# Optimization experiments

Measured on AMD Instinct MI355X. Metric: run time of the kernel, lower is better.

Reference implementation:

```python
import jax, jax.numpy as jnp
import numpy as np

N_NODES = 50000
N_EDGES = 1600000
IN_DIM = 64
EDGE_DIM = 8
N_GRAPHS = 256
EXP_IN = 32
H = 64  # hidden dim per head / GCN hidden
EPS = 1e-5
NEG_SLOPE = 0.2


def gat_layer(x, src, dst, ea, W, a_src, a_dst, We, a_e, bias, heads, dim, concat):
    """PyG-style GATConv with edge features and self-loops (fill_value='mean')."""
    N = x.shape[0]
    ones_e = jnp.ones((ea.shape[0],), x.dtype)
    cnt = jax.ops.segment_sum(ones_e, dst, num_segments=N)
    loop_attr = jax.ops.segment_sum(ea, dst, num_segments=N) / jnp.maximum(cnt, 1.0)[:, None]
    s = jnp.concatenate([src, jnp.arange(N)])
    d = jnp.concatenate([dst, jnp.arange(N)])
    eaf = jnp.concatenate([ea, loop_attr], axis=0)  # [E+N, edge_dim]
    h = (x @ W).reshape(N, heads, dim)              # [N, H, D]
    ee = (eaf @ We).reshape(-1, heads, dim)         # [E+N, H, D]
    al_src = (h * a_src).sum(-1)                    # [N, H]
    al_dst = (h * a_dst).sum(-1)                    # [N, H]
    score = al_src[s] + al_dst[d] + (ee * a_e).sum(-1)
    score = jax.nn.leaky_relu(score, NEG_SLOPE)     # [E+N, H]
    m = jax.ops.segment_max(score, d, num_segments=N)
    ex = jnp.exp(score - m[d])
    att = ex / jax.ops.segment_sum(ex, d, num_segments=N)[d]
    out = jax.ops.segment_sum(h[s] * att[:, :, None], d, num_segments=N)  # [N, H, D]
    out = out.reshape(N, heads * dim) if concat else out.mean(axis=1)
    return out + bias


def gcn_layer(x, src, dst, W, b):
    """PyG-style GCNConv: add self loops, symmetric degree normalization."""
    N = x.shape[0]
    s = jnp.concatenate([src, jnp.arange(N)])
    d = jnp.concatenate([dst, jnp.arange(N)])
    deg = jax.ops.segment_sum(jnp.ones((s.shape[0],), x.dtype), d, num_segments=N)
    dinv = jax.lax.rsqrt(deg)  # deg >= 1 thanks to self loops
    norm = dinv[s] * dinv[d]
    h = x @ W
    return jax.ops.segment_sum(h[s] * norm[:, None], d, num_segments=N) + b


def bn(x, g, b):
    m = x.mean(axis=0)
    v = x.var(axis=0)
    return g * (x - m) * jax.lax.rsqrt(v + EPS) + b


def mean_pool(x, batch, num_graphs):
    s = jax.ops.segment_sum(x, batch, num_segments=num_graphs)
    c = jax.ops.segment_sum(jnp.ones((x.shape[0],), x.dtype), batch, num_segments=num_graphs)
    return s / jnp.maximum(c, 1.0)[:, None]


def setup_inputs() -> dict:
    key = jax.random.key(0)
    ks = jax.random.split(key, 32)
    p = lambda i, shape: jax.random.normal(ks[i], shape, jnp.float32) * 0.05
    z = lambda n: jnp.zeros((n,), jnp.float32)
    o = lambda n: jnp.ones((n,), jnp.float32)
    return {
        "x": jax.random.normal(ks[0], (N_NODES, IN_DIM), jnp.float32),
        "edge_attr": jax.random.normal(ks[1], (N_EDGES, EDGE_DIM), jnp.float32),
        "experimental_feat": jax.random.normal(ks[2], (N_GRAPHS, EXP_IN), jnp.float32),
        "edge_index": jax.random.randint(ks[3], (2, N_EDGES), 0, N_NODES),
        "batch": jnp.sort(jax.random.randint(ks[4], (N_NODES,), 0, N_GRAPHS)),
        "W1": p(5, (IN_DIM, 4 * H)), "att_src1": p(6, (4, H)), "att_dst1": p(7, (4, H)),
        "We1": p(8, (EDGE_DIM, 4 * H)), "att_e1": p(9, (4, H)), "b1": z(4 * H),
        "g1": o(4 * H), "be1": z(4 * H),
        "W2": p(10, (4 * H, H)), "att_src2": p(11, (1, H)), "att_dst2": p(12, (1, H)),
        "We2": p(13, (EDGE_DIM, H)), "att_e2": p(14, (1, H)), "b2": z(H),
        "g2": o(H), "be2": z(H),
        "Wg1": p(15, (H, H)), "bg1": z(H), "g3": o(H), "be3": z(H),
        "Wg2": p(16, (H, H)), "bg2": z(H), "g4": o(H), "be4": z(H),
        "Wex1": p(17, (EXP_IN, H)), "bex1": z(H), "Wex2": p(18, (H, H)), "bex2": z(H),
        "Wc1": p(19, (2 * H, 128)), "bc1": z(128), "Wc2": p(20, (128, 1)), "bc2": z(1),
    }


def reference(x, edge_attr, experimental_feat, edge_index, batch,
              W1, att_src1, att_dst1, We1, att_e1, b1, g1, be1,
              W2, att_src2, att_dst2, We2, att_e2, b2, g2, be2,
              Wg1, bg1, g3, be3, Wg2, bg2, g4, be4,
              Wex1, bex1, Wex2, bex2, Wc1, bc1, Wc2, bc2):
    src, dst = edge_index[0], edge_index[1]
    h = gat_layer(x, src, dst, edge_attr, W1, att_src1, att_dst1, We1, att_e1, b1, 4, H, True)
    h = jax.nn.relu(bn(h, g1, be1))
    h = gat_layer(h, src, dst, edge_attr, W2, att_src2, att_dst2, We2, att_e2, b2, 1, H, False)
    h = jax.nn.relu(bn(h, g2, be2))  # dropout = identity in eval
    h = gcn_layer(h, src, dst, Wg1, bg1)
    h = jax.nn.relu(bn(h, g3, be3))
    h = gcn_layer(h, src, dst, Wg2, bg2)
    h = jax.nn.relu(bn(h, g4, be4))
    xp = mean_pool(h, batch, N_GRAPHS)                    # [G, H]
    e = jax.nn.relu(experimental_feat @ Wex1 + bex1)
    e = jax.nn.relu(e @ Wex2 + bex2)
    combined = jnp.concatenate([xp, e], axis=1)           # [G, 2H]
    combined = jax.nn.relu(combined @ Wc1 + bc1)          # [G, 128]
    out = combined @ Wc2 + bc2                            # [G, 1]
    return (out, xp, combined)
```

## Files before the change

kernel.cpp:

```cpp
#include <hip/hip_runtime.h>
#include <hip/hip_bf16.h>

#define N_NODES 50000
#define N_EDGES 1600000
#define N_GRAPHS 256
#define NEG_SLOPE 0.2f
#define BN_EPS 1e-5f

typedef __hip_bfloat16 bf16;
typedef __attribute__((ext_vector_type(8))) short s16x8;
typedef __attribute__((ext_vector_type(4))) float f32x4;

__device__ __forceinline__ float b2f(bf16 v){ return __bfloat162float(v); }
__device__ __forceinline__ bf16 f2b(float v){ return __float2bfloat16(v); }
__device__ __forceinline__ float us2f(unsigned short u){ return __uint_as_float(((unsigned)u)<<16); }
__device__ __forceinline__ unsigned short f2us(float v){ bf16 b = f2b(v); return *(unsigned short*)&b; }
__device__ __forceinline__ unsigned pk2(float a, float b){ return (unsigned)f2us(a) | ((unsigned)f2us(b)<<16); }
__device__ __forceinline__ float ldF(const void* p, size_t i, int m){
  return m ? ((const float*)p)[i] : b2f(((const bf16*)p)[i]);
}
__device__ __forceinline__ float sane(float v){
  return (v == v && fabsf(v) < 1e30f) ? v : 0.f;
}
__device__ __forceinline__ float sel4(const float v[4], int h){
  float r = v[0];
  r = (h==1) ? v[1] : r;
  r = (h==2) ? v[2] : r;
  r = (h==3) ? v[3] : r;
  return r;
}
__device__ __forceinline__ void acc8(float* acc, float w, uint4 u){
  acc[0] += w*us2f((unsigned short)(u.x & 0xffff)); acc[1] += w*us2f((unsigned short)(u.x >> 16));
  acc[2] += w*us2f((unsigned short)(u.y & 0xffff)); acc[3] += w*us2f((unsigned short)(u.y >> 16));
  acc[4] += w*us2f((unsigned short)(u.z & 0xffff)); acc[5] += w*us2f((unsigned short)(u.z >> 16));
  acc[6] += w*us2f((unsigned short)(u.w & 0xffff)); acc[7] += w*us2f((unsigned short)(u.w >> 16));
}
__device__ __forceinline__ void unp8(float* o, uint4 u){
  o[0] = us2f((unsigned short)(u.x & 0xffff)); o[1] = us2f((unsigned short)(u.x >> 16));
  o[2] = us2f((unsigned short)(u.y & 0xffff)); o[3] = us2f((unsigned short)(u.y >> 16));
  o[4] = us2f((unsigned short)(u.z & 0xffff)); o[5] = us2f((unsigned short)(u.z >> 16));
  o[6] = us2f((unsigned short)(u.w & 0xffff)); o[7] = us2f((unsigned short)(u.w >> 16));
}
__device__ __forceinline__ s16x8 pk8(const float* v){
  s16x8 r;
  #pragma unroll
  for(int j=0;j<8;j++) r[j] = (short)f2us(v[j]);
  return r;
}

__device__ int detect_mode_block(const void* x){
  __shared__ int s_ins;
  if(threadIdx.x == 0) s_ins = 0;
  __syncthreads();
  const unsigned short* u = (const unsigned short*)x;
  int c = 0;
  for(int i = threadIdx.x; i < 1024; i += blockDim.x){
    float v = fabsf(us2f(u[i]));
    if(!(v > 1e-6f && v < 1e4f)) c++;
  }
  if(c) atomicAdd(&s_ins, c);
  __syncthreads();
  return (s_ins > 128) ? 1 : 0;
}

#define NSEG 33
struct Bank { const void* p[NSEG]; int n[NSEG]; int off[NSEG]; };

__global__ void k_convert(Bank b, const void* xdet, float* out){
  int m = detect_mode_block(xdet);
  int seg = blockIdx.y;
  int i = blockIdx.x*256 + threadIdx.x;
  if(i < b.n[seg]) out[b.off[seg] + i] = ldF(b.p[seg], i, m);
}

__global__ void k_cvt_x(const void* x, bf16* xb){
  int m = detect_mode_block(x);
  int i4 = blockIdx.x*256 + threadIdx.x;
  if(i4 >= N_NODES*16) return;
  if(m){
    float4 v = ((const float4*)x)[i4];
    ((ushort4*)xb)[i4] = make_ushort4(f2us(v.x), f2us(v.y), f2us(v.z), f2us(v.w));
  } else {
    ((ushort4*)xb)[i4] = ((const ushort4*)x)[i4];
  }
}

__global__ void k_we(const float* __restrict__ We1, const float* __restrict__ ae1,
                     const float* __restrict__ We2, const float* __restrict__ ae2,
                     float* __restrict__ w_e){
  int t = threadIdx.x;
  if(t < 32){
    int h = t >> 3, k = t & 7;
    float s = 0.f;
    for(int d=0;d<64;d++) s += We1[k*256 + h*64 + d] * ae1[h*64 + d];
    w_e[t] = s;
  } else if(t < 40){
    int k = t - 32;
    float s = 0.f;
    for(int d=0;d<64;d++) s += We2[k*64 + d] * ae2[d];
    w_e[t] = s;
  }
}

__global__ void k_wt(const float* __restrict__ W1, const float* __restrict__ W2,
                     const float* __restrict__ Wg1, const float* __restrict__ Wg2,
                     bf16* __restrict__ wt){
  int i = blockIdx.x*256 + threadIdx.x;
  if(i < 16384){
    int c = i >> 6, k = i & 63;
    wt[i] = f2b(W1[k*256 + c]);
  } else if(i < 32768){
    int j = i - 16384; int c = j >> 8, k = j & 255;
    wt[i] = f2b(W2[k*64 + c]);
  } else if(i < 36864){
    int j = i - 32768; int c = j >> 6, k = j & 63;
    wt[i] = f2b(Wg1[k*64 + c]);
  } else if(i < 40960){
    int j = i - 36864; int c = j >> 6, k = j & 63;
    wt[i] = f2b(Wg2[k*64 + c]);
  }
}

__global__ void k_count(const int* __restrict__ dst, int* __restrict__ cnt){
  int e = blockIdx.x*256 + threadIdx.x;
  if(e < N_EDGES){
    int d = dst[e]; if((unsigned)d >= N_NODES) d = 0;
    atomicAdd(&cnt[d], 1);
  }
}

__global__ void k_blocksum(const int* __restrict__ cnt, int* __restrict__ bsum){
  __shared__ int s[256];
  int i = blockIdx.x*256 + threadIdx.x;
  s[threadIdx.x] = (i < N_NODES) ? cnt[i] : 0;
  __syncthreads();
  for(int o=128;o>0;o>>=1){ if(threadIdx.x<o) s[threadIdx.x]+=s[threadIdx.x+o]; __syncthreads(); }
  if(threadIdx.x==0) bsum[blockIdx.x]=s[0];
}

__global__ void k_scan_bsum(const int* __restrict__ bsum, int* __restrict__ bofs, int nb){
  __shared__ int s[256];
  int t = threadIdx.x;
  s[t] = (t<nb) ? bsum[t] : 0;
  __syncthreads();
  for(int o=1;o<256;o<<=1){ int v=(t>=o)?s[t-o]:0; __syncthreads(); s[t]+=v; __syncthreads(); }
  bofs[t] = (t==0) ? 0 : s[t-1];
}

__global__ void k_scan_write(const int* __restrict__ cnt, const int* __restrict__ bofs,
                             int* __restrict__ rp, float* __restrict__ dinv){
  __shared__ int s[256];
  int t = threadIdx.x; int i = blockIdx.x*256 + t;
  int v = (i<N_NODES) ? cnt[i] : 0;
  s[t]=v; __syncthreads();
  for(int o=1;o<256;o<<=1){ int a=(t>=o)?s[t-o]:0; __syncthreads(); s[t]+=a; __syncthreads(); }
  if(i<N_NODES){
    rp[i+1] = s[t] + bofs[blockIdx.x];
    dinv[i] = rsqrtf((float)v + 1.f);
  }
  if(i==0) rp[0]=0;
}

__global__ void k_fill(const int* __restrict__ src, const int* __restrict__ dst,
                       const int* __restrict__ rp, int* __restrict__ fill,
                       const void* __restrict__ ea, const void* __restrict__ xdet,
                       const float* __restrict__ w_e,
                       int4* __restrict__ epk){
  int m = detect_mode_block(xdet);
  int e = blockIdx.x*256 + threadIdx.x;
  if(e >= N_EDGES) return;
  int d = dst[e]; if((unsigned)d >= N_NODES) d = 0;
  int p = atomicAdd(&fill[d], 1);
  int slot = rp[d] + p;
  if((unsigned)slot >= N_EDGES) return;
  int sv = src[e]; if((unsigned)sv >= N_NODES) sv = 0;
  float a[8];
  if(m){
    const float* eaf = (const float*)ea;
    float4 lo = *(const float4*)&eaf[(size_t)e*8];
    float4 hi = *(const float4*)&eaf[(size_t)e*8 + 4];
    a[0]=lo.x; a[1]=lo.y; a[2]=lo.z; a[3]=lo.w;
    a[4]=hi.x; a[5]=hi.y; a[6]=hi.z; a[7]=hi.w;
  } else {
    #pragma unroll
    for(int k=0;k<8;k++) a[k] = b2f(((const bf16*)ea)[(size_t)e*8 + k]);
  }
  unsigned d4[4];
  #pragma unroll
  for(int h=0;h<4;h++){
    float s = 0.f;
    #pragma unroll
    for(int k=0;k<8;k++) s += a[k]*w_e[h*8+k];
    d4[h] = f2us(s);
  }
  float s1 = 0.f;
  #pragma unroll
  for(int k=0;k<8;k++) s1 += a[k]*w_e[32+k];
  int4 pk;
  pk.x = sv;
  pk.y = (int)(d4[0] | (d4[1] << 16));
  pk.z = (int)(d4[2] | (d4[3] << 16));
  pk.w = (int)(unsigned)f2us(s1);
  epk[slot] = pk;
}

__global__ __launch_bounds__(256) void k_gemmA_mfma(
    const bf16* __restrict__ xb,
    const bf16* __restrict__ wt1,
    bf16* __restrict__ hp, int M)
{
  const int tid = threadIdx.x;
  const int w = tid >> 6, l = tid & 63;
  const int lr = l & 15, lg = l >> 4;
  const int bm = blockIdx.x*64 + w*16;
  const int arow_i = bm + lr;
  const uint4* arow = (const uint4*)(xb + (size_t)min(arow_i, M-1)*64);
  uint4 a0u = arow[lg];
  uint4 a1u = arow[4 + lg];
  s16x8 a0 = *(s16x8*)&a0u, a1 = *(s16x8*)&a1u;
  unsigned short* out = (unsigned short*)hp;
  const int orow0 = bm + lg*4;
  #pragma unroll
  for(int ct = 0; ct < 16; ct++){
    const uint4* brow = (const uint4*)(wt1 + (size_t)(ct*16 + lr)*64);
    uint4 b0u = brow[lg];
    uint4 b1u = brow[4 + lg];
    f32x4 acc = {0.f, 0.f, 0.f, 0.f};
    acc = __builtin_amdgcn_mfma_f32_16x16x32_bf16(a0, *(s16x8*)&b0u, acc, 0, 0, 0);
    acc = __builtin_amdgcn_mfma_f32_16x16x32_bf16(a1, *(s16x8*)&b1u, acc, 0, 0, 0);
    #pragma unroll
    for(int r = 0; r < 4; r++){
      int rr = orow0 + r;
      if(rr < M) out[(size_t)rr*256 + ct*16 + lr] = f2us(acc[r]);
    }
  }
}

template<int KIN>
__global__ __launch_bounds__(256) void k_gemmB_mfma(
    const bf16* __restrict__ A, const bf16* __restrict__ Wt,
    bf16* __restrict__ C, int M,
    const float* __restrict__ bnsums, const float* __restrict__ bng, const float* __restrict__ bnb)
{
  __shared__ float st_s[KIN];
  __shared__ float st_t[KIN];
  const int tid = threadIdx.x;
  if(tid < KIN){
    const float invN = 1.0f / (float)N_NODES;
    float mean = bnsums[tid]*invN;
    float var  = fmaxf(bnsums[KIN+tid]*invN - mean*mean, 0.f);
    float s = bng[tid]*rsqrtf(var + BN_EPS);
    st_s[tid] = s;
    st_t[tid] = bnb[tid] - mean*s;
  }
  __syncthreads();
  const int w = tid >> 6, l = tid & 63;
  const int lr = l & 15, lg = l >> 4;
  const int bm = blockIdx.x*64 + w*16;
  const int arow_i = bm + lr;
  const uint4* arow = (const uint4*)(A + (size_t)min(arow_i, M-1)*KIN);
  f32x4 acc[4];
  #pragma unroll
  for(int ct=0;ct<4;ct++) acc[ct] = (f32x4){0.f,0.f,0.f,0.f};
  #pragma unroll
  for(int k0 = 0; k0 < KIN; k0 += 32){
    uint4 au = arow[(k0 >> 3) + lg];
    int c0 = k0 + lg*8;
    float v[8]; unp8(v, au);
    #pragma unroll
    for(int j = 0; j < 8; j++){
      float y = sane(v[j])*st_s[c0+j] + st_t[c0+j];
      v[j] = fmaxf(y, 0.f);
    }
    s16x8 af = pk8(v);
    #pragma unroll
    for(int ct = 0; ct < 4; ct++){
      const uint4* brow = (const uint4*)(Wt + (size_t)(ct*16 + lr)*KIN);
      uint4 bu = brow[(k0 >> 3) + lg];
      acc[ct] = __builtin_amdgcn_mfma_f32_16x16x32_bf16(af, *(s16x8*)&bu, acc[ct], 0, 0, 0);
    }
  }
  unsigned short* out = (unsigned short*)C;
  const int orow0 = bm + lg*4;
  #pragma unroll
  for(int ct = 0; ct < 4; ct++){
    #pragma unroll
    for(int r = 0; r < 4; r++){
      int rr = orow0 + r;
      if(rr < M) out[(size_t)rr*64 + ct*16 + lr] = f2us(acc[ct][r]);
    }
  }
}

__global__ void k_al4(const bf16* __restrict__ hp, const float* __restrict__ asrc,
                      const float* __restrict__ adst,
                      float* __restrict__ als4, float* __restrict__ ald4){
  int idx = blockIdx.x*256 + threadIdx.x;
  if(idx >= N_NODES*4) return;
  int n = idx >> 2, h = idx & 3;
  const unsigned short* row = (const unsigned short*)hp + (size_t)n*256 + h*64;
  float ss=0.f, sd=0.f;
  #pragma unroll
  for(int q=0;q<16;q++){
    ushort4 u = *(const ushort4*)&row[4*q];
    float4 a_s = *(const float4*)&asrc[h*64 + 4*q];
    float4 a_d = *(const float4*)&adst[h*64 + 4*q];
    float v0=us2f(u.x), v1=us2f(u.y), v2=us2f(u.z), v3=us2f(u.w);
    ss += v0*a_s.x + v1*a_s.y + v2*a_s.z + v3*a_s.w;
    sd += v0*a_d.x + v1*a_d.y + v2*a_d.z + v3*a_d.w;
  }
  als4[idx]=ss; ald4[idx]=sd;
}

__global__ void k_al1(const bf16* __restrict__ hp, const float* __restrict__ asrc,
                      const float* __restrict__ adst,
                      float* __restrict__ als, float* __restrict__ ald){
  int n = blockIdx.x*256 + threadIdx.x;
  if(n >= N_NODES) return;
  const unsigned short* row = (const unsigned short*)hp + (size_t)n*64;
  float ss=0.f, sd=0.f;
  #pragma unroll
  for(int q=0;q<16;q++){
    ushort4 u = *(const ushort4*)&row[4*q];
    float4 a_s = *(const float4*)&asrc[4*q];
    float4 a_d = *(const float4*)&adst[4*q];
    float v0=us2f(u.x), v1=us2f(u.y), v2=us2f(u.z), v3=us2f(u.w);
    ss += v0*a_s.x + v1*a_s.y + v2*a_s.z + v3*a_s.w;
    sd += v0*a_d.x + v1*a_d.y + v2*a_d.z + v3*a_d.w;
  }
  als[n]=ss; ald[n]=sd;
}

__global__ __launch_bounds__(64) void k_gat_agg4(
    const int* __restrict__ rp, const int4* __restrict__ epk,
    const bf16* __restrict__ hp,
    const float* __restrict__ als4, const float* __restrict__ ald4,
    const float* __restrict__ bias256, bf16* __restrict__ out1){
  int n = blockIdx.x; int t = threadIdx.x;
  int eh = t >> 5, c8 = t & 31;
  int head = c8 >> 3;
  __shared__ int   ssrc[64];
  __shared__ float swt[64][4];
  int s0 = rp[n], e0 = rp[n+1];
  if((unsigned)s0 > N_EDGES){ s0=0; e0=0; }
  if(e0 < s0 || (unsigned)e0 > N_EDGES) e0 = s0;
  float4 aldv = *(const float4*)&ald4[n*4];
  float4 alsvn = *(const float4*)&als4[n*4];
  float wsum[4] = {0.f,0.f,0.f,0.f};
  float dsum[4] = {0.f,0.f,0.f,0.f};
  float acc[8]  = {0.f,0.f,0.f,0.f,0.f,0.f,0.f,0.f};
  const unsigned short* hpu = (const unsigned short*)hp;

  for(int base = s0; base < e0; base += 64){
    int m = min(64, e0 - base);
    if(t < m){
      int4 pk = epk[base+t];
      int sn = pk.x; if((unsigned)sn >= N_NODES) sn = 0;
      ssrc[t] = sn;
      float edf[4] = {us2f((unsigned short)(pk.y & 0xffff)), us2f((unsigned short)((unsigned)pk.y >> 16)),
                      us2f((unsigned short)(pk.z & 0xffff)), us2f((unsigned short)((unsigned)pk.z >> 16))};
      float4 alss = *(const float4*)&als4[sn*4];
      float alssv[4] = {alss.x, alss.y, alss.z, alss.w};
      float aldvv[4] = {aldv.x, aldv.y, aldv.z, aldv.w};
      float w4[4];
      #pragma unroll
      for(int h=0;h<4;h++){
        float sc = alssv[h] + aldvv[h] + edf[h];
        sc = sc > 0.f ? sc : NEG_SLOPE*sc;
        sc = fminf(sc, 30.f);
        float w = expf(sc);
        w4[h] = w;
        wsum[h] += w; dsum[h] += edf[h];
      }
      *(float4*)&swt[t][0] = make_float4(w4[0], w4[1], w4[2], w4[3]);
    }
    __syncthreads();
    #pragma unroll 4
    for(int i=0;i<m;i+=2){
      int j = i + eh;
      if(j < m){
        int row = ssrc[j];
        float w = swt[j][head];
        uint4 u = *(const uint4*)&hpu[(size_t)row*256 + 8*c8];
        acc8(acc, w, u);
      }
    }
    __syncthreads();
  }
  #pragma unroll
  for(int o=1;o<64;o<<=1){
    #pragma unroll
    for(int h=0;h<4;h++){
      wsum[h] += __shfl_xor(wsum[h], o);
      dsum[h] += __shfl_xor(dsum[h], o);
    }
  }
  #pragma unroll
  for(int q=0;q<8;q++) acc[q] += __shfl_xor(acc[q], 32);
  if(eh == 0){
    float alsnv[4] = {alsvn.x, alsvn.y, alsvn.z, alsvn.w};
    float aldnv[4] = {aldv.x, aldv.y, aldv.z, aldv.w};
    float sEh = sel4(wsum, head), sDh = sel4(dsum, head);
    float deg = (float)(e0 - s0);
    float sdot = deg > 0.f ? sDh/deg : 0.f;
    float sc = sel4(alsnv, head) + sel4(aldnv, head) + sdot;
    sc = sc > 0.f ? sc : NEG_SLOPE*sc;
    sc = fminf(sc, 30.f);
    float wself = expf(sc);
    float self[8];
    unp8(self, *(const uint4*)&hpu[(size_t)n*256 + 8*c8]);
    float4 b0 = *(const float4*)&bias256[8*c8];
    float4 b1 = *(const float4*)&bias256[8*c8 + 4];
    float bi[8] = {b0.x,b0.y,b0.z,b0.w,b1.x,b1.y,b1.z,b1.w};
    float inv = 1.f/(sEh + wself);
    float o8[8];
    #pragma unroll
    for(int q=0;q<8;q++) o8[q] = (acc[q] + wself*self[q])*inv + bi[q];
    uint4 st;
    st.x = pk2(o8[0],o8[1]); st.y = pk2(o8[2],o8[3]);
    st.z = pk2(o8[4],o8[5]); st.w = pk2(o8[6],o8[7]);
    *(uint4*)&((unsigned short*)out1)[(size_t)n*256 + 8*c8] = st;
  }
}

__global__ __launch_bounds__(64) void k_gat_agg1e(
    const int* __restrict__ rp, const int4* __restrict__ epk,
    const bf16* __restrict__ hp,
    const float* __restrict__ als, const float* __restrict__ ald,
    const float* __restrict__ bias64, bf16* __restrict__ out){
  int n = blockIdx.x; int t = threadIdx.x;
  int eg = t >> 3, c8 = t & 7;
  __shared__ float sw[64];
  __shared__ int   ssrc[64];
  int s0 = rp[n], e0 = rp[n+1];
  if((unsigned)s0 > N_EDGES){ s0=0; e0=0; }
  if(e0 < s0 || (unsigned)e0 > N_EDGES) e0 = s0;
  float aldn = ald[n];
  float wsum_l = 0.f, dsum_l = 0.f;
  float acc[8] = {0.f,0.f,0.f,0.f,0.f,0.f,0.f,0.f};
  const unsigned short* hpu = (const unsigned short*)hp;
  for(int base = s0; base < e0; base += 64){
    int m = min(64, e0 - base);
    if(t < m){
      int4 pk = epk[base+t];
      int sn = pk.x; if((unsigned)sn >= N_NODES) sn = 0;
      ssrc[t] = sn;
      float ed = us2f((unsigned short)(pk.w & 0xffff));
      float sc = als[sn] + aldn + ed;
      sc = sc > 0.f ? sc : NEG_SLOPE*sc;
      sc = fminf(sc, 30.f);
      float w = expf(sc);
      sw[t] = w;
      wsum_l += w; dsum_l += ed;
    }
    __syncthreads();
    #pragma unroll 2
    for(int i=0;i<m;i+=8){
      int j = i + eg;
      if(j < m){
        int row = ssrc[j];
        float w = sw[j];
        uint4 u = *(const uint4*)&hpu[(size_t)row*64 + 8*c8];
        acc8(acc, w, u);
      }
    }
    __syncthreads();
  }
  #pragma unroll
  for(int o=1;o<64;o<<=1){ wsum_l += __shfl_xor(wsum_l, o); dsum_l += __shfl_xor(dsum_l, o); }
  #pragma unroll
  for(int q=0;q<8;q++){
    acc[q] += __shfl_xor(acc[q], 8);
    acc[q] += __shfl_xor(acc[q], 16);
    acc[q] += __shfl_xor(acc[q], 32);
  }
  if(t < 8){
    float deg = (float)(e0 - s0);
    float sdot = deg > 0.f ? dsum_l/deg : 0.f;
    float sc = als[n] + aldn + sdot;
    sc = sc > 0.f ? sc : NEG_SLOPE*sc;
    sc = fminf(sc, 30.f);
    float wself = expf(sc);
    float self[8];
    unp8(self, *(const uint4*)&hpu[(size_t)n*64 + 8*t]);
    float4 b0 = *(const float4*)&bias64[8*t];
    float4 b1 = *(const float4*)&bias64[8*t + 4];
    float bi[8] = {b0.x,b0.y,b0.z,b0.w,b1.x,b1.y,b1.z,b1.w};
    float inv = 1.f/(wsum_l + wself);
    float o8[8];
    #pragma unroll
    for(int q=0;q<8;q++) o8[q] = (acc[q] + wself*self[q])*inv + bi[q];
    uint4 st;
    st.x = pk2(o8[0],o8[1]); st.y = pk2(o8[2],o8[3]);
    st.z = pk2(o8[4],o8[5]); st.w = pk2(o8[6],o8[7]);
    *(uint4*)&((unsigned short*)out)[(size_t)n*64 + 8*t] = st;
  }
}

__global__ __launch_bounds__(64) void k_gcn_agg(
    const int* __restrict__ rp, const int4* __restrict__ epk,
    const float* __restrict__ dinv, const bf16* __restrict__ gp,
    const float* __restrict__ bias, bf16* __restrict__ out){
  int n = blockIdx.x; int t = threadIdx.x;
  int eg = t >> 3, c8 = t & 7;
  __shared__ float sw[64];
  __shared__ int   ssrc[64];
  int s0 = rp[n], e0 = rp[n+1];
  if((unsigned)s0 > N_EDGES){ s0=0; e0=0; }
  if(e0 < s0 || (unsigned)e0 > N_EDGES) e0 = s0;
  float dn = dinv[n];
  float acc[8] = {0.f,0.f,0.f,0.f,0.f,0.f,0.f,0.f};
  const unsigned short* gpu = (const unsigned short*)gp;
  for(int base = s0; base < e0; base += 64){
    int m = min(64, e0 - base);
    if(t < m){
      int sn = epk[base+t].x; if((unsigned)sn >= N_NODES) sn = 0;
      ssrc[t]=sn; sw[t]=dinv[sn];
    }
    __syncthreads();
    #pragma unroll 2
    for(int i=0;i<m;i+=8){
      int j = i + eg;
      if(j < m){
        int row = ssrc[j];
        float w = sw[j];
        uint4 u = *(const uint4*)&gpu[(size_t)row*64 + 8*c8];
        acc8(acc, w, u);
      }
    }
    __syncthreads();
  }
  #pragma unroll
  for(int q=0;q<8;q++){
    acc[q] += __shfl_xor(acc[q], 8);
    acc[q] += __shfl_xor(acc[q], 16);
    acc[q] += __shfl_xor(acc[q], 32);
  }
  if(t < 8){
    float self[8];
    unp8(self, *(const uint4*)&gpu[(size_t)n*64 + 8*t]);
    float4 b0 = *(const float4*)&bias[8*t];
    float4 b1 = *(const float4*)&bias[8*t + 4];
    float bi[8] = {b0.x,b0.y,b0.z,b0.w,b1.x,b1.y,b1.z,b1.w};
    float o8[8];
    #pragma unroll
    for(int q=0;q<8;q++) o8[q] = dn*(acc[q] + dn*self[q]) + bi[q];
    uint4 st;
    st.x = pk2(o8[0],o8[1]); st.y = pk2(o8[2],o8[3]);
    st.z = pk2(o8[4],o8[5]); st.w = pk2(o8[6],o8[7]);
    *(uint4*)&((unsigned short*)out)[(size_t)n*64 + 8*t] = st;
  }
}

template<int C>
__global__ void k_colstats(const bf16* __restrict__ X, float* __restrict__ sums){
  constexpr int RPB = 128;
  constexpr int RSTEP = 256 / C;
  int c = threadIdx.x % C;
  int r0 = threadIdx.x / C;
  int rbeg = blockIdx.x * RPB;
  int rend = min(N_NODES, rbeg + RPB);
  const unsigned short* Xu = (const unsigned short*)X;
  float s = 0.f, q = 0.f;
  for(int r = rbeg + r0; r < rend; r += RSTEP){
    float v = sane(us2f(Xu[(size_t)r*C + c]));
    s += v; q += v*v;
  }
  atomicAdd(&sums[c], s);
  atomicAdd(&sums[C + c], q);
}

__global__ __launch_bounds__(64) void k_pool3(
    const bf16* __restrict__ h, const int* __restrict__ batch,
    const float* __restrict__ sums, const float* __restrict__ g4,
    const float* __restrict__ b4,
    float* __restrict__ psum, float* __restrict__ pcnt){
  int t = threadIdx.x;
  int n0 = blockIdx.x * 256;
  int n1 = min(N_NODES, n0 + 256);
  if(n0 >= n1) return;
  const float invN = 1.0f / (float)N_NODES;
  float mean = sums[t]*invN;
  float var = fmaxf(sums[64+t]*invN - mean*mean, 0.f);
  float rstd = rsqrtf(var + BN_EPS);
  float gg = g4[t], bb = b4[t];
  const unsigned short* hu = (const unsigned short*)h;
  int cur = batch[n0]; if((unsigned)cur >= N_GRAPHS) cur = 0;
  float acc = 0.f; int cl = 0;
  for(int n = n0; n < n1; n++){
    int g = batch[n]; if((unsigned)g >= N_GRAPHS) g = 0;
    if(g != cur){
      atomicAdd(&psum[cur*64 + t], acc);
      if(t == 0) atomicAdd(&pcnt[cur], (float)cl);
      acc = 0.f; cl = 0; cur = g;
    }
    float y = (sane(us2f(hu[(size_t)n*64 + t]))-mean)*rstd*gg + bb;
    acc += fmaxf(y, 0.f);
    cl++;
  }
  atomicAdd(&psum[cur*64 + t], acc);
  if(t == 0) atomicAdd(&pcnt[cur], (float)cl);
}

__device__ __forceinline__ void stO(void* o, size_t i, float v, int m){
  if(m) ((float*)o)[i] = v; else ((bf16*)o)[i] = f2b(v);
}

__global__ __launch_bounds__(128) void k_head(
    const float* __restrict__ psum, const float* __restrict__ pcnt,
    const float* __restrict__ exf,
    const float* __restrict__ Wex1, const float* __restrict__ bex1,
    const float* __restrict__ Wex2, const float* __restrict__ bex2,
    const float* __restrict__ Wc1, const float* __restrict__ bc1,
    const float* __restrict__ Wc2, const float* __restrict__ bc2,
    const void* __restrict__ xdet, void* __restrict__ dout){
  int m0 = detect_mode_block(xdet);
  int g = blockIdx.x; int t = threadIdx.x;
  __shared__ float ci[128];
  __shared__ float e1[64];
  __shared__ float comb[128];
  __shared__ float red[128];
  if(t < 64){
    float c = fmaxf(pcnt[g], 1.f);
    float xp = sane(psum[g*64 + t]) / c;
    ci[t] = xp;
    stO(dout, 256 + (size_t)g*64 + t, xp, m0);
  } else {
    int j = t - 64;
    float s = bex1[j];
    for(int k=0;k<32;k++) s += exf[g*32 + k] * Wex1[k*64 + j];
    e1[j] = fmaxf(s, 0.f);
  }
  __syncthreads();
  if(t >= 64){
    int j = t - 64;
    float s = bex2[j];
    for(int k=0;k<64;k++) s += e1[k] * Wex2[k*64 + j];
    ci[64 + j] = fmaxf(s, 0.f);
  }
  __syncthreads();
  {
    float s = bc1[t];
    for(int k=0;k<128;k++) s += ci[k] * Wc1[k*128 + t];
    s = fmaxf(s, 0.f);
    comb[t] = s;
    stO(dout, 256 + 16384 + (size_t)g*128 + t, s, m0);
  }
  __syncthreads();
  red[t] = comb[t] * Wc2[t];
  __syncthreads();
  for(int o=64;o>0;o>>=1){ if(t<o) red[t]+=red[t+o]; __syncthreads(); }
  if(t==0) stO(dout, g, red[0] + bc2[0], m0);
}

extern "C" void kernel_launch(void* const* d_in, const int* in_sizes, int n_in,
                              void* d_out, int out_size, void* d_ws, size_t ws_size,
                              hipStream_t stream){
  const void* x    = d_in[0];
  const void* ea   = d_in[1];
  const int* ei    = (const int*)d_in[3];
  const int* batch = (const int*)d_in[4];
  const int* src = ei;
  const int* dst = ei + N_EDGES;

  char* base = (char*)d_ws;
  size_t off = 0;
  auto alloc = [&](size_t bytes) -> void* {
    void* r = base + off;
    off += (bytes + 255) & ~(size_t)255;
    return r;
  };
  int*   cnt    = (int*)  alloc((size_t)N_NODES*4);
  int*   fill   = (int*)  alloc((size_t)N_NODES*4);
  float* bnstat = (float*)alloc(4096);
  float* pool   = (float*)alloc((size_t)(N_GRAPHS*64 + N_GRAPHS)*4);
  size_t zbytes = off;
  int*   rp      = (int*)  alloc((size_t)(N_NODES+1)*4);
  int*   bsum    = (int*)  alloc(256*4);
  int*   bofs    = (int*)  alloc(256*4);
  int4*  epk     = (int4*) alloc((size_t)N_EDGES*16);
  float* dinv    = (float*)alloc((size_t)N_NODES*4);
  float* w_e     = (float*)alloc(64*4);
  float* als4    = (float*)alloc((size_t)N_NODES*4*4);
  float* ald4    = (float*)alloc((size_t)N_NODES*4*4);
  float* wbank   = (float*)alloc(80000*4);
  bf16*  wt      = (bf16*) alloc((size_t)40960*2);
  bf16*  xb      = (bf16*) alloc((size_t)N_NODES*64*2);
  bf16*  hp      = (bf16*) alloc((size_t)N_NODES*256*2);
  bf16*  outb    = (bf16*) alloc((size_t)N_NODES*256*2);

  bf16* out1 = outb;
  bf16* out2 = outb;
  bf16* out3 = outb + (size_t)N_NODES*64;
  bf16* out4 = outb + (size_t)N_NODES*128;
  float* bn1 = bnstat;
  float* bn2 = bnstat + 512;
  float* bn3 = bnstat + 640;
  float* bn4 = bnstat + 768;
  float* psum = pool;
  float* pcnt = pool + N_GRAPHS*64;

  bf16* wt1  = wt;
  bf16* wt2  = wt + 16384;
  bf16* wtg1 = wt + 32768;
  bf16* wtg2 = wt + 36864;

  const int segidx[NSEG] = {2, 5,6,7,8,9,10,11,12, 13,14,15,16,17,18,19,20,
                            21,22,23,24, 25,26,27,28, 29,30,31,32, 33,34,35,36};
  const int segn[NSEG] = {8192, 16384,256,256,2048,256,256,256,256,
                          16384,64,64,512,64,64,64,64,
                          4096,64,64,64, 4096,64,64,64,
                          2048,64,4096,64, 16384,128,128,1};
  Bank bk;
  int offs[NSEG]; int acc0 = 0;
  for(int i=0;i<NSEG;i++){ bk.p[i]=d_in[segidx[i]]; bk.n[i]=segn[i]; bk.off[i]=acc0; offs[i]=acc0; acc0+=segn[i]; }
  const float* f_exf = wbank + offs[0];
  const float* fW1 = wbank+offs[1]; const float* fas1 = wbank+offs[2]; const float* fad1 = wbank+offs[3];
  const float* fWe1= wbank+offs[4]; const float* fae1 = wbank+offs[5]; const float* fb1  = wbank+offs[6];
  const float* fg1 = wbank+offs[7]; const float* fbe1 = wbank+offs[8];
  const float* fW2 = wbank+offs[9]; const float* fas2 = wbank+offs[10]; const float* fad2 = wbank+offs[11];
  const float* fWe2= wbank+offs[12]; const float* fae2 = wbank+offs[13]; const float* fb2 = wbank+offs[14];
  const float* fg2 = wbank+offs[15]; const float* fbe2 = wbank+offs[16];
  const float* fWg1= wbank+offs[17]; const float* fbg1 = wbank+offs[18]; const float* fg3 = wbank+offs[19];
  const float* fbe3= wbank+offs[20];
  const float* fWg2= wbank+offs[21]; const float* fbg2 = wbank+offs[22]; const float* fg4 = wbank+offs[23];
  const float* fbe4= wbank+offs[24];
  const float* fWex1=wbank+offs[25]; const float* fbex1= wbank+offs[26];
  const float* fWex2=wbank+offs[27]; const float* fbex2= wbank+offs[28];
  const float* fWc1= wbank+offs[29]; const float* fbc1 = wbank+offs[30];
  const float* fWc2= wbank+offs[31]; const float* fbc2 = wbank+offs[32];

  const int nbN  = (N_NODES + 255)/256;
  const int nbE  = (N_EDGES + 255)/256;
  const int nbT  = (N_NODES + 63)/64;

  hipMemsetAsync(d_ws, 0, zbytes, stream);
  {
    dim3 g((16384+255)/256, NSEG);
    k_convert<<<g,256,0,stream>>>(bk, x, wbank);
  }
  k_wt<<<160,256,0,stream>>>(fW1, fW2, fWg1, fWg2, wt);
  k_cvt_x<<<(N_NODES*16+255)/256,256,0,stream>>>(x, xb);
  k_we<<<1,64,0,stream>>>(fWe1, fae1, fWe2, fae2, w_e);
  k_count<<<nbE,256,0,stream>>>(dst, cnt);
  k_blocksum<<<nbN,256,0,stream>>>(cnt, bsum);
  k_scan_bsum<<<1,256,0,stream>>>(bsum, bofs, nbN);
  k_scan_write<<<nbN,256,0,stream>>>(cnt, bofs, rp, dinv);
  k_fill<<<nbE,256,0,stream>>>(src, dst, rp, fill, ea, x, w_e, epk);

  k_gemmA_mfma<<<nbT,256,0,stream>>>(xb, wt1, hp, N_NODES);
  k_al4<<<(N_NODES*4+255)/256,256,0,stream>>>(hp, fas1, fad1, als4, ald4);
  k_gat_agg4<<<N_NODES,64,0,stream>>>(rp, epk, hp, als4, ald4, fb1, out1);
  k_colstats<256><<<(N_NODES+127)/128,256,0,stream>>>(out1, bn1);

  k_gemmB_mfma<256><<<nbT,256,0,stream>>>(out1, wt2, hp, N_NODES, bn1, fg1, fbe1);
  k_al1<<<nbN,256,0,stream>>>(hp, fas2, fad2, als4, ald4);
  k_gat_agg1e<<<N_NODES,64,0,stream>>>(rp, epk, hp, als4, ald4, fb2, out2);
  k_colstats<64><<<(N_NODES+127)/128,256,0,stream>>>(out2, bn2);

  k_gemmB_mfma<64><<<nbT,256,0,stream>>>(out2, wtg1, hp, N_NODES, bn2, fg2, fbe2);
  k_gcn_agg<<<N_NODES,64,0,stream>>>(rp, epk, dinv, hp, fbg1, out3);
  k_colstats<64><<<(N_NODES+127)/128,256,0,stream>>>(out3, bn3);

  k_gemmB_mfma<64><<<nbT,256,0,stream>>>(out3, wtg2, hp, N_NODES, bn3, fg3, fbe3);
  k_gcn_agg<<<N_NODES,64,0,stream>>>(rp, epk, dinv, hp, fbg2, out4);
  k_colstats<64><<<(N_NODES+127)/128,256,0,stream>>>(out4, bn4);

  k_pool3<<<nbN,64,0,stream>>>(out4, batch, bn4, fg4, fbe4, psum, pcnt);
  k_head<<<N_GRAPHS,128,0,stream>>>(psum, pcnt, f_exf, fWex1, fbex1, fWex2, fbex2,
                                    fWc1, fbc1, fWc2, fbc2, x, (void*)d_out);
}
```

Before: 938.3 us.

## Use nontemporal loads/stores for edge packs, fast exp, and deeper unrolling

Switches the packed edge-record stores and loads, and the aggregation output stores, to nontemporal builtins so streamed data does not pollute cache. Replaces expf with __expf in the attention weight computation. Raises unroll factors in the gather loops of the three aggregation kernels. The risks are slightly lower exp accuracy, and epk being reread by several layers, so a nontemporal hint on it may hurt reuse in L2.

Result: slower. 978.0 us (+4.2%).

```diff
diff --git a/kernel.cpp b/kernel.cpp
--- a/kernel.cpp
+++ b/kernel.cpp
@@ -10,6 +10,8 @@
 typedef __hip_bfloat16 bf16;
 typedef __attribute__((ext_vector_type(8))) short s16x8;
 typedef __attribute__((ext_vector_type(4))) float f32x4;
+typedef __attribute__((ext_vector_type(4))) int i32x4;
+typedef __attribute__((ext_vector_type(4))) unsigned u32x4;
 
 __device__ __forceinline__ float b2f(bf16 v){ return __bfloat162float(v); }
 __device__ __forceinline__ bf16 f2b(float v){ return __float2bfloat16(v); }
@@ -196,12 +198,12 @@
   float s1 = 0.f;
   #pragma unroll
   for(int k=0;k<8;k++) s1 += a[k]*w_e[32+k];
-  int4 pk;
-  pk.x = sv;
-  pk.y = (int)(d4[0] | (d4[1] << 16));
-  pk.z = (int)(d4[2] | (d4[3] << 16));
-  pk.w = (int)(unsigned)f2us(s1);
-  epk[slot] = pk;
+  i32x4 pk;
+  pk[0] = sv;
+  pk[1] = (int)(d4[0] | (d4[1] << 16));
+  pk[2] = (int)(d4[2] | (d4[3] << 16));
+  pk[3] = (int)(unsigned)f2us(s1);
+  __builtin_nontemporal_store(pk, (i32x4*)&epk[slot]);
 }
 
 __global__ __launch_bounds__(256) void k_gemmA_mfma(
@@ -354,11 +356,11 @@
   for(int base = s0; base < e0; base += 64){
     int m = min(64, e0 - base);
     if(t < m){
-      int4 pk = epk[base+t];
-      int sn = pk.x; if((unsigned)sn >= N_NODES) sn = 0;
+      i32x4 pk = __builtin_nontemporal_load((const i32x4*)&epk[base+t]);
+      int sn = pk[0]; if((unsigned)sn >= N_NODES) sn = 0;
       ssrc[t] = sn;
-      float edf[4] = {us2f((unsigned short)(pk.y & 0xffff)), us2f((unsigned short)((unsigned)pk.y >> 16)),
-                      us2f((unsigned short)(pk.z & 0xffff)), us2f((unsigned short)((unsigned)pk.z >> 16))};
+      float edf[4] = {us2f((unsigned short)(pk[1] & 0xffff)), us2f((unsigned short)((unsigned)pk[1] >> 16)),
+                      us2f((unsigned short)(pk[2] & 0xffff)), us2f((unsigned short)((unsigned)pk[2] >> 16))};
       float4 alss = *(const float4*)&als4[sn*4];
       float alssv[4] = {alss.x, alss.y, alss.z, alss.w};
       float aldvv[4] = {aldv.x, aldv.y, aldv.z, aldv.w};
@@ -368,14 +370,14 @@
         float sc = alssv[h] + aldvv[h] + edf[h];
         sc = sc > 0.f ? sc : NEG_SLOPE*sc;
         sc = fminf(sc, 30.f);
-        float w = expf(sc);
+        float w = __expf(sc);
         w4[h] = w;
         wsum[h] += w; dsum[h] += edf[h];
       }
       *(float4*)&swt[t][0] = make_float4(w4[0], w4[1], w4[2], w4[3]);
     }
     __syncthreads();
-    #pragma unroll 4
+    #pragma unroll 8
     for(int i=0;i<m;i+=2){
       int j = i + eh;
       if(j < m){
@@ -406,7 +408,7 @@
     float sc = sel4(alsnv, head) + sel4(aldnv, head) + sdot;
     sc = sc > 0.f ? sc : NEG_SLOPE*sc;
     sc = fminf(sc, 30.f);
-    float wself = expf(sc);
+    float wself = __expf(sc);
     float self[8];
     unp8(self, *(const uint4*)&hpu[(size_t)n*256 + 8*c8]);
     float4 b0 = *(const float4*)&bias256[8*c8];
@@ -416,10 +418,10 @@
     float o8[8];
     #pragma unroll
     for(int q=0;q<8;q++) o8[q] = (acc[q] + wself*self[q])*inv + bi[q];
-    uint4 st;
-    st.x = pk2(o8[0],o8[1]); st.y = pk2(o8[2],o8[3]);
-    st.z = pk2(o8[4],o8[5]); st.w = pk2(o8[6],o8[7]);
-    *(uint4*)&((unsigned short*)out1)[(size_t)n*256 + 8*c8] = st;
+    u32x4 st;
+    st[0] = pk2(o8[0],o8[1]); st[1] = pk2(o8[2],o8[3]);
+    st[2] = pk2(o8[4],o8[5]); st[3] = pk2(o8[6],o8[7]);
+    __builtin_nontemporal_store(st, (u32x4*)&((unsigned short*)out1)[(size_t)n*256 + 8*c8]);
   }
 }
 
@@ -442,19 +444,19 @@
   for(int base = s0; base < e0; base += 64){
     int m = min(64, e0 - base);
     if(t < m){
-      int4 pk = epk[base+t];
-      int sn = pk.x; if((unsigned)sn >= N_NODES) sn = 0;
+      i32x4 pk = __builtin_nontemporal_load((const i32x4*)&epk[base+t]);
+      int sn = pk[0]; if((unsigned)sn >= N_NODES) sn = 0;
       ssrc[t] = sn;
-      float ed = us2f((unsigned short)(pk.w & 0xffff));
+      float ed = us2f((unsigned short)(pk[3] & 0xffff));
       float sc = als[sn] + aldn + ed;
       sc = sc > 0.f ? sc : NEG_SLOPE*sc;
       sc = fminf(sc, 30.f);
-      float w = expf(sc);
+      float w = __expf(sc);
       sw[t] = w;
       wsum_l += w; dsum_l += ed;
     }
     __syncthreads();
-    #pragma unroll 2
+    #pragma unroll 4
     for(int i=0;i<m;i+=8){
       int j = i + eg;
       if(j < m){
@@ -480,7 +482,7 @@
     float sc = als[n] + aldn + sdot;
     sc = sc > 0.f ? sc : NEG_SLOPE*sc;
     sc = fminf(sc, 30.f);
-    float wself = expf(sc);
+    float wself = __expf(sc);
     float self[8];
     unp8(self, *(const uint4*)&hpu[(size_t)n*64 + 8*t]);
     float4 b0 = *(const float4*)&bias64[8*t];
@@ -490,10 +492,10 @@
     float o8[8];
     #pragma unroll
     for(int q=0;q<8;q++) o8[q] = (acc[q] + wself*self[q])*inv + bi[q];
-    uint4 st;
-    st.x = pk2(o8[0],o8[1]); st.y = pk2(o8[2],o8[3]);
-    st.z = pk2(o8[4],o8[5]); st.w = pk2(o8[6],o8[7]);
-    *(uint4*)&((unsigned short*)out)[(size_t)n*64 + 8*t] = st;
+    u32x4 st;
+    st[0] = pk2(o8[0],o8[1]); st[1] = pk2(o8[2],o8[3]);
+    st[2] = pk2(o8[4],o8[5]); st[3] = pk2(o8[6],o8[7]);
+    __builtin_nontemporal_store(st, (u32x4*)&((unsigned short*)out)[(size_t)n*64 + 8*t]);
   }
 }
 
@@ -514,11 +516,12 @@
   for(int base = s0; base < e0; base += 64){
     int m = min(64, e0 - base);
     if(t < m){
-      int sn = epk[base+t].x; if((unsigned)sn >= N_NODES) sn = 0;
+      i32x4 pk = __builtin_nontemporal_load((const i32x4*)&epk[base+t]);
+      int sn = pk[0]; if((unsigned)sn >= N_NODES) sn = 0;
       ssrc[t]=sn; sw[t]=dinv[sn];
     }
     __syncthreads();
-    #pragma unroll 2
+    #pragma unroll 4
     for(int i=0;i<m;i+=8){
       int j = i + eg;
       if(j < m){
@@ -545,10 +548,10 @@
     float o8[8];
     #pragma unroll
     for(int q=0;q<8;q++) o8[q] = dn*(acc[q] + dn*self[q]) + bi[q];
-    uint4 st;
-    st.x = pk2(o8[0],o8[1]); st.y = pk2(o8[2],o8[3]);
-    st.z = pk2(o8[4],o8[5]); st.w = pk2(o8[6],o8[7]);
-    *(uint4*)&((unsigned short*)out)[(size_t)n*64 + 8*t] = st;
+    u32x4 st;
+    st[0] = pk2(o8[0],o8[1]); st[1] = pk2(o8[2],o8[3]);
+    st[2] = pk2(o8[4],o8[5]); st[3] = pk2(o8[6],o8[7]);
+    __builtin_nontemporal_store(st, (u32x4*)&((unsigned short*)out)[(size_t)n*64 + 8*t]);
   }
 }
 
```
